# Kernel optimization log

Hardware: AMD Instinct MI355X
Metric: run time of the kernel (lower is better)

## Reference

```python
import jax, jax.numpy as jnp
import numpy as np

B, CIN, COUT = 2, 64, 64
D, H, W = 8, 32, 32
KD = KH = KW = 3
K = KD * KH * KW  # 27
STRIDE, PAD, DIL = 1, 1, 1
DOUT = (D + 2 * PAD - DIL * (KD - 1) - 1) // STRIDE + 1
HOUT = (H + 2 * PAD - DIL * (KH - 1) - 1) // STRIDE + 1
WOUT = (W + 2 * PAD - DIL * (KW - 1) - 1) // STRIDE + 1


def setup_inputs() -> dict:
    key = jax.random.key(0)
    k1, k2, k3, k4 = jax.random.split(key, 4)
    x = jax.random.normal(k1, (B, CIN, D, H, W), dtype=jnp.float32)
    offset = jax.random.normal(k2, (B, 3 * K, DOUT, HOUT, WOUT), dtype=jnp.float32)
    weight = jax.random.normal(k3, (COUT, CIN, KD, KH, KW), dtype=jnp.float32) * 0.05
    bias = jax.random.normal(k4, (COUT,), dtype=jnp.float32) * 0.1
    return {"x": x, "offset": offset, "weight": weight, "bias": bias}


def _trilinear_sample(xb, zd, zh, zw):
    # xb: [C, D, H, W]; zd/zh/zw: [K, P] float sampling coords (zero padding outside)
    Dd, Hh, Ww = xb.shape[1], xb.shape[2], xb.shape[3]
    d0 = jnp.floor(zd); h0 = jnp.floor(zh); w0 = jnp.floor(zw)
    fd = zd - d0; fh = zh - h0; fw = zw - w0
    d0i = d0.astype(jnp.int32); h0i = h0.astype(jnp.int32); w0i = w0.astype(jnp.int32)
    acc = jnp.zeros((xb.shape[0],) + zd.shape, dtype=xb.dtype)
    for dd in (0, 1):
        for dh in (0, 1):
            for dw in (0, 1):
                di = d0i + dd; hi = h0i + dh; wi = w0i + dw
                wgt = ((fd if dd else 1.0 - fd) * (fh if dh else 1.0 - fh)
                       * (fw if dw else 1.0 - fw))
                valid = ((di >= 0) & (di < Dd) & (hi >= 0) & (hi < Hh)
                         & (wi >= 0) & (wi < Ww)).astype(xb.dtype)
                v = xb[:, jnp.clip(di, 0, Dd - 1), jnp.clip(hi, 0, Hh - 1),
                       jnp.clip(wi, 0, Ww - 1)]  # [C, K, P]
                acc = acc + v * (wgt * valid)[None]
    return acc


def _deform_conv3d(x, offset, weight, bias):
    Bb = x.shape[0]
    P = DOUT * HOUT * WOUT
    # kernel taps
    kd, kh, kw = jnp.unravel_index(jnp.arange(K), (KD, KH, KW))
    # output grid
    od, oh, ow = jnp.meshgrid(jnp.arange(DOUT), jnp.arange(HOUT), jnp.arange(WOUT), indexing="ij")
    base_d = (od[None] * STRIDE - PAD + kd[:, None, None, None] * DIL).astype(jnp.float32)  # [K,Do,Ho,Wo]
    base_h = (oh[None] * STRIDE - PAD + kh[:, None, None, None] * DIL).astype(jnp.float32)
    base_w = (ow[None] * STRIDE - PAD + kw[:, None, None, None] * DIL).astype(jnp.float32)
    off = offset.reshape(Bb, K, 3, DOUT, HOUT, WOUT)  # per-tap (dd, dh, dw)
    zd = (base_d[None] + off[:, :, 0]).reshape(Bb, K, P)
    zh = (base_h[None] + off[:, :, 1]).reshape(Bb, K, P)
    zw = (base_w[None] + off[:, :, 2]).reshape(Bb, K, P)
    sampled = jax.vmap(_trilinear_sample)(x, zd, zh, zw)  # [B, C, K, P]
    wmat = weight.reshape(COUT, CIN, K)
    out = jnp.einsum("bckp,ock->bop", sampled, wmat)  # [B, COUT, P]
    out = out + bias[None, :, None]
    return out.reshape(Bb, COUT, DOUT, HOUT, WOUT)


def reference(x, offset, weight, bias):
    return _deform_conv3d(x, offset, weight, bias)
```

## Files before the change

### kernel.cpp

```cpp
#include <hip/hip_runtime.h>
#include <hip/hip_bf16.h>


#define BB    2
#define CINC  64
#define COUTC 64
#define DDEP  8
#define HGT   32
#define WID   32
#define KK    27
#define KGRP  3
#define KPG   9
#define KPH   3
#define PP    8192
#define TP    64
#define LDW   72

typedef short s16x8 __attribute__((ext_vector_type(8)));
typedef float f32x4 __attribute__((ext_vector_type(4)));

__device__ __forceinline__ unsigned short f2bf(float f) {
    unsigned u = __builtin_bit_cast(unsigned, f);
    u += 0x7FFFu + ((u >> 16) & 1u);
    return (unsigned short)(u >> 16);
}

__device__ __forceinline__ unsigned pack2bf(float lo, float hi) {
    return (unsigned)f2bf(lo) | ((unsigned)f2bf(hi) << 16);
}

__device__ __forceinline__ float bfu_lo(unsigned v) {
    return __builtin_bit_cast(float, v << 16);
}
__device__ __forceinline__ float bfu_hi(unsigned v) {
    return __builtin_bit_cast(float, v & 0xFFFF0000u);
}

__global__ void pre_kernel(const float* __restrict__ x, const float* __restrict__ w,
                           unsigned short* __restrict__ xt, unsigned short* __restrict__ wt) {
    __shared__ float sT[64][65];
    const int t    = threadIdx.x;
    const int lane = t & 63;
    const int wv   = t >> 6;
    const int half = lane >> 5;
    const int c2   = lane & 31;
    int blk = blockIdx.x;
    if (blk < 256) {
        int b  = blk >> 7;
        int s0 = (blk & 127) * 64;
        #pragma unroll
        for (int i = 0; i < 16; ++i) {
            int c = wv * 16 + i;
            sT[c][lane] = x[(size_t)(b * CINC + c) * PP + s0 + lane];
        }
        __syncthreads();
        #pragma unroll
        for (int i = 0; i < 8; ++i) {
            int s = wv * 16 + 2 * i + half;
            unsigned pk = pack2bf(sT[2 * c2][s], sT[2 * c2 + 1][s]);
            *(unsigned*)&xt[(size_t)(b * PP + s0 + s) * 64 + 2 * c2] = pk;
        }
    } else {
        int id = (blk - 256) * 256 + t;
        if (id < KK * COUTC * CINC) {
            int c = id & 63;
            int o = (id >> 6) & 63;
            int k = id >> 12;
            wt[id] = f2bf(w[(o * CINC + c) * KK + k]);
        }
    }
}

__global__ __launch_bounds__(256, 3) void deform_kernel(
    const unsigned short* __restrict__ xt, const float* __restrict__ off,
    const unsigned short* __restrict__ wt, const float* __restrict__ bias,
    float* __restrict__ out)
{
    __shared__ unsigned short sW[KPH * COUTC * LDW] __attribute__((aligned(16)));
    __shared__ unsigned short sS[TP * LDW]          __attribute__((aligned(16)));
    __shared__ int   sIdx[KPH][TP][8] __attribute__((aligned(16)));
    __shared__ float sCf[KPH][TP][8]  __attribute__((aligned(16)));

    const int t    = threadIdx.x;
    const int lane = t & 63;
    const int wv   = t >> 6;
    const int half = lane >> 5;
    const int c2   = lane & 31;
    const int b    = blockIdx.x >> 7;
    const int p0   = (blockIdx.x & 127) * TP;
    const int kg   = blockIdx.y;

    const unsigned short* xb = xt + (size_t)b * PP * 64;

    f32x4 acc[4];
    #pragma unroll
    for (int f = 0; f < 4; ++f) acc[f] = (f32x4)0.0f;

    const int n0 = lane & 15;
    const int q  = lane >> 4;

    #pragma unroll 1
    for (int ph = 0; ph < 3; ++ph) {
        const int kbase = kg * KPG + ph * KPH;

        const unsigned short* wk = wt + kbase * (COUTC * CINC);
        #pragma unroll
        for (int j = 0; j < 6; ++j) {
            int idx = j * 2048 + t * 8;
            int kl  = idx >> 12;
            int rem = idx & 4095;
            *(s16x8*)&sW[kl * (COUTC * LDW) + (rem >> 6) * LDW + (rem & 63)] =
                *(const s16x8*)(wk + idx);
        }

        if (t < KPH * TP) {
            int kl = t >> 6;
            int k  = kbase + kl;
            int pl = t & 63;
            int pp = p0 + pl;
            int ow = pp & 31;
            int oh = (pp >> 5) & 31;
            int od = pp >> 10;
            int kd = k / 9;
            int kh = (k - kd * 9) / 3;
            int kw = k - kd * 9 - kh * 3;
            const float* ob = off + (size_t)(b * (3 * KK) + 3 * k) * PP + pp;
            float zd = (float)(od - 1 + kd) + ob[0];
            float zh = (float)(oh - 1 + kh) + ob[PP];
            float zw = (float)(ow - 1 + kw) + ob[2 * PP];

            float fdf = floorf(zd); int d0 = (int)fdf; float fd = zd - fdf;
            float fhf = floorf(zh); int h0 = (int)fhf; float fh = zh - fhf;
            float fwf = floorf(zw); int w0 = (int)fwf; float fw = zw - fwf;

            float Bd0 = (d0 >= 0     && d0 < DDEP)     ? 1.0f - fd : 0.0f;
            float Bd1 = (d0 + 1 >= 0 && d0 + 1 < DDEP) ? fd        : 0.0f;
            float Ch0 = (h0 >= 0     && h0 < HGT)      ? 1.0f - fh : 0.0f;
            float Ch1 = (h0 + 1 >= 0 && h0 + 1 < HGT)  ? fh        : 0.0f;
            float Aw0 = (w0 >= 0     && w0 < WID)      ? 1.0f - fw : 0.0f;
            float Aw1 = (w0 + 1 >= 0 && w0 + 1 < WID)  ? fw        : 0.0f;
            int dc0 = min(max(d0, 0), DDEP - 1);
            int dc1 = min(max(d0 + 1, 0), DDEP - 1);
            int hc0 = min(max(h0, 0), HGT - 1);
            int hc1 = min(max(h0 + 1, 0), HGT - 1);
            int wc0 = min(max(w0, 0), WID - 1);
            int wc1 = min(max(w0 + 1, 0), WID - 1);

            int dhb0 = (dc0 * HGT + hc0) * (WID * 64);
            int dhb1 = (dc0 * HGT + hc1) * (WID * 64);
            int dhb2 = (dc1 * HGT + hc0) * (WID * 64);
            int dhb3 = (dc1 * HGT + hc1) * (WID * 64);
            int wo0 = wc0 * 64, wo1 = wc1 * 64;
            sIdx[kl][pl][0] = dhb0 + wo0;
            sIdx[kl][pl][1] = dhb1 + wo0;
            sIdx[kl][pl][2] = dhb2 + wo0;
            sIdx[kl][pl][3] = dhb3 + wo0;
            sIdx[kl][pl][4] = dhb0 + wo1;
            sIdx[kl][pl][5] = dhb1 + wo1;
            sIdx[kl][pl][6] = dhb2 + wo1;
            sIdx[kl][pl][7] = dhb3 + wo1;
            float bc0 = Bd0 * Ch0, bc1 = Bd0 * Ch1, bc2 = Bd1 * Ch0, bc3 = Bd1 * Ch1;
            sCf[kl][pl][0] = bc0 * Aw0;
            sCf[kl][pl][1] = bc1 * Aw0;
            sCf[kl][pl][2] = bc2 * Aw0;
            sCf[kl][pl][3] = bc3 * Aw0;
            sCf[kl][pl][4] = bc0 * Aw1;
            sCf[kl][pl][5] = bc1 * Aw1;
            sCf[kl][pl][6] = bc2 * Aw1;
            sCf[kl][pl][7] = bc3 * Aw1;
        }
        __syncthreads();

        #pragma unroll
        for (int kl = 0; kl < KPH; ++kl) {
            #pragma unroll
            for (int jp = 0; jp < 8; ++jp) {
                int prow = wv * 16 + 2 * jp + half;
                const int4   i0 = *(const int4*)&sIdx[kl][prow][0];
                const int4   i1 = *(const int4*)&sIdx[kl][prow][4];
                const float4 u0 = *(const float4*)&sCf[kl][prow][0];
                const float4 u1 = *(const float4*)&sCf[kl][prow][4];
                float slo = 0.0f, shi = 0.0f;
                {
                    unsigned v0 = *(const unsigned*)(xb + i0.x + 2 * c2);
                    unsigned v1 = *(const unsigned*)(xb + i0.y + 2 * c2);
                    unsigned v2 = *(const unsigned*)(xb + i0.z + 2 * c2);
                    unsigned v3 = *(const unsigned*)(xb + i0.w + 2 * c2);
                    unsigned v4 = *(const unsigned*)(xb + i1.x + 2 * c2);
                    unsigned v5 = *(const unsigned*)(xb + i1.y + 2 * c2);
                    unsigned v6 = *(const unsigned*)(xb + i1.z + 2 * c2);
                    unsigned v7 = *(const unsigned*)(xb + i1.w + 2 * c2);
                    slo += u0.x * bfu_lo(v0); shi += u0.x * bfu_hi(v0);
                    slo += u0.y * bfu_lo(v1); shi += u0.y * bfu_hi(v1);
                    slo += u0.z * bfu_lo(v2); shi += u0.z * bfu_hi(v2);
                    slo += u0.w * bfu_lo(v3); shi += u0.w * bfu_hi(v3);
                    slo += u1.x * bfu_lo(v4); shi += u1.x * bfu_hi(v4);
                    slo += u1.y * bfu_lo(v5); shi += u1.y * bfu_hi(v5);
                    slo += u1.z * bfu_lo(v6); shi += u1.z * bfu_hi(v6);
                    slo += u1.w * bfu_lo(v7); shi += u1.w * bfu_hi(v7);
                }
                *(unsigned*)&sS[prow * LDW + 2 * c2] = pack2bf(slo, shi);
            }
            __syncthreads();

            {
                const unsigned short* sWk = &sW[kl * (COUTC * LDW)];
                s16x8 a0 = *(const s16x8*)&sWk[(16 * wv + n0) * LDW +      8 * q];
                s16x8 a1 = *(const s16x8*)&sWk[(16 * wv + n0) * LDW + 32 + 8 * q];
                #pragma unroll
                for (int f = 0; f < 4; ++f) {
                    s16x8 b0 = *(const s16x8*)&sS[(16 * f + n0) * LDW +      8 * q];
                    s16x8 b1 = *(const s16x8*)&sS[(16 * f + n0) * LDW + 32 + 8 * q];
                    acc[f] = __builtin_amdgcn_mfma_f32_16x16x32_bf16(a0, b0, acc[f], 0, 0, 0);
                    acc[f] = __builtin_amdgcn_mfma_f32_16x16x32_bf16(a1, b1, acc[f], 0, 0, 0);
                }
            }
            __syncthreads();
        }
    }

    float bv[4];
    #pragma unroll
    for (int r = 0; r < 4; ++r) bv[r] = (kg == 0) ? bias[16 * wv + 4 * q + r] : 0.0f;
    #pragma unroll
    for (int f = 0; f < 4; ++f) {
        #pragma unroll
        for (int r = 0; r < 4; ++r) {
            int o = 16 * wv + 4 * q + r;
            int p = p0 + 16 * f + n0;
            unsafeAtomicAdd(&out[(size_t)(b * COUTC + o) * PP + p], acc[f][r] + bv[r]);
        }
    }
}

extern "C" void kernel_launch(void* const* d_in, const int* in_sizes, int n_in,
                              void* d_out, int out_size, void* d_ws, size_t ws_size,
                              hipStream_t stream) {
    const float* x    = (const float*)d_in[0];
    const float* off  = (const float*)d_in[1];
    const float* w    = (const float*)d_in[2];
    const float* bias = (const float*)d_in[3];
    float* out        = (float*)d_out;

    unsigned short* xt = (unsigned short*)d_ws;
    unsigned short* wt = (unsigned short*)((char*)d_ws + (size_t)BB * PP * 64 * 2);

    (void)hipMemsetAsync(out, 0, (size_t)out_size * sizeof(float), stream);
    hipLaunchKernelGGL(pre_kernel, dim3(256 + (KK * COUTC * CINC + 255) / 256), dim3(256), 0,
                       stream, x, w, xt, wt);
    hipLaunchKernelGGL(deform_kernel, dim3(BB * (PP / TP), KGRP), dim3(256), 0, stream,
                       xt, off, wt, bias, out);
}
```

Baseline: 103.3 us.

## Make sampling and MFMA wave-local, drop barriers, fold output zeroing into prekernel

Each wave now computes the offset coefficients, the trilinear samples and the MFMA for its own 16 output points, looping over all output-channel groups. The intra-phase __syncthreads between the sampling stage and the MFMA stage are removed; one barrier at the top of each phase still protects the weight reload. The separate hipMemsetAsync is replaced by extra zeroing blocks in pre_kernel. Sampling uses packed f32x2 math and a v_cvt_pk_bf16_f32 instruction, and the MFMA section is wrapped in s_setprio. The risk is that sW A-fragment LDS reads per MFMA rise, and the coefficient stage leaves a quarter of the lanes idle.

```diff
diff --git a/kernel.cpp b/kernel.cpp
--- a/kernel.cpp
+++ b/kernel.cpp
@@ -18,6 +18,7 @@
 
 typedef short s16x8 __attribute__((ext_vector_type(8)));
 typedef float f32x4 __attribute__((ext_vector_type(4)));
+typedef float f32x2 __attribute__((ext_vector_type(2)));
 
 __device__ __forceinline__ unsigned short f2bf(float f) {
     unsigned u = __builtin_bit_cast(unsigned, f);
@@ -29,15 +30,18 @@
     return (unsigned)f2bf(lo) | ((unsigned)f2bf(hi) << 16);
 }
 
-__device__ __forceinline__ float bfu_lo(unsigned v) {
-    return __builtin_bit_cast(float, v << 16);
-}
-__device__ __forceinline__ float bfu_hi(unsigned v) {
-    return __builtin_bit_cast(float, v & 0xFFFF0000u);
-}
-
+__device__ __forceinline__ f32x2 up2(unsigned v) {
+    f32x2 r;
+    r.x = __builtin_bit_cast(float, v << 16);
+    r.y = __builtin_bit_cast(float, v & 0xFFFF0000u);
+    return r;
+}
+
+#define WBLOCKS 432
+#define ZBLOCKS 1024
 __global__ void pre_kernel(const float* __restrict__ x, const float* __restrict__ w,
-                           unsigned short* __restrict__ xt, unsigned short* __restrict__ wt) {
+                           unsigned short* __restrict__ xt, unsigned short* __restrict__ wt,
+                           float* __restrict__ out) {
     __shared__ float sT[64][65];
     const int t    = threadIdx.x;
     const int lane = t & 63;
@@ -60,7 +64,7 @@
             unsigned pk = pack2bf(sT[2 * c2][s], sT[2 * c2 + 1][s]);
             *(unsigned*)&xt[(size_t)(b * PP + s0 + s) * 64 + 2 * c2] = pk;
         }
-    } else {
+    } else if (blk < 256 + WBLOCKS) {
         int id = (blk - 256) * 256 + t;
         if (id < KK * COUTC * CINC) {
             int c = id & 63;
@@ -68,6 +72,9 @@
             int k = id >> 12;
             wt[id] = f2bf(w[(o * CINC + c) * KK + k]);
         }
+    } else {
+        int id = (blk - 256 - WBLOCKS) * 256 + t;
+        ((float4*)out)[id] = make_float4(0.f, 0.f, 0.f, 0.f);
     }
 }
 
@@ -90,18 +97,23 @@
     const int p0   = (blockIdx.x & 127) * TP;
     const int kg   = blockIdx.y;
 
-    const unsigned short* xb = xt + (size_t)b * PP * 64;
+    const unsigned short* xb  = xt + (size_t)b * PP * 64;
+    const unsigned short* xbl = xb + 2 * c2;
 
     f32x4 acc[4];
     #pragma unroll
-    for (int f = 0; f < 4; ++f) acc[f] = (f32x4)0.0f;
-
-    const int n0 = lane & 15;
-    const int q  = lane >> 4;
+    for (int g = 0; g < 4; ++g) acc[g] = (f32x4)0.0f;
+
+    const int n0  = lane & 15;
+    const int q   = lane >> 4;
+    const int cr  = lane & 15;
+    const int ckl = lane >> 4;
 
     #pragma unroll 1
     for (int ph = 0; ph < 3; ++ph) {
         const int kbase = kg * KPG + ph * KPH;
+
+        __syncthreads();
 
         const unsigned short* wk = wt + kbase * (COUTC * CINC);
         #pragma unroll
@@ -113,10 +125,9 @@
                 *(const s16x8*)(wk + idx);
         }
 
-        if (t < KPH * TP) {
-            int kl = t >> 6;
-            int k  = kbase + kl;
-            int pl = t & 63;
+        if (ckl < KPH) {
+            int k  = kbase + ckl;
+            int pl = 16 * wv + cr;
             int pp = p0 + pl;
             int ow = pp & 31;
             int oh = (pp >> 5) & 31;
@@ -151,23 +162,23 @@
             int dhb2 = (dc1 * HGT + hc0) * (WID * 64);
             int dhb3 = (dc1 * HGT + hc1) * (WID * 64);
             int wo0 = wc0 * 64, wo1 = wc1 * 64;
-            sIdx[kl][pl][0] = dhb0 + wo0;
-            sIdx[kl][pl][1] = dhb1 + wo0;
-            sIdx[kl][pl][2] = dhb2 + wo0;
-            sIdx[kl][pl][3] = dhb3 + wo0;
-            sIdx[kl][pl][4] = dhb0 + wo1;
-            sIdx[kl][pl][5] = dhb1 + wo1;
-            sIdx[kl][pl][6] = dhb2 + wo1;
-            sIdx[kl][pl][7] = dhb3 + wo1;
+            sIdx[ckl][pl][0] = dhb0 + wo0;
+            sIdx[ckl][pl][1] = dhb1 + wo0;
+            sIdx[ckl][pl][2] = dhb2 + wo0;
+            sIdx[ckl][pl][3] = dhb3 + wo0;
+            sIdx[ckl][pl][4] = dhb0 + wo1;
+            sIdx[ckl][pl][5] = dhb1 + wo1;
+            sIdx[ckl][pl][6] = dhb2 + wo1;
+            sIdx[ckl][pl][7] = dhb3 + wo1;
             float bc0 = Bd0 * Ch0, bc1 = Bd0 * Ch1, bc2 = Bd1 * Ch0, bc3 = Bd1 * Ch1;
-            sCf[kl][pl][0] = bc0 * Aw0;
-            sCf[kl][pl][1] = bc1 * Aw0;
-            sCf[kl][pl][2] = bc2 * Aw0;
-            sCf[kl][pl][3] = bc3 * Aw0;
-            sCf[kl][pl][4] = bc0 * Aw1;
-            sCf[kl][pl][5] = bc1 * Aw1;
-            sCf[kl][pl][6] = bc2 * Aw1;
-            sCf[kl][pl][7] = bc3 * Aw1;
+            sCf[ckl][pl][0] = bc0 * Aw0;
+            sCf[ckl][pl][1] = bc1 * Aw0;
+            sCf[ckl][pl][2] = bc2 * Aw0;
+            sCf[ckl][pl][3] = bc3 * Aw0;
+            sCf[ckl][pl][4] = bc0 * Aw1;
+            sCf[ckl][pl][5] = bc1 * Aw1;
+            sCf[ckl][pl][6] = bc2 * Aw1;
+            sCf[ckl][pl][7] = bc3 * Aw1;
         }
         __syncthreads();
 
@@ -175,60 +186,59 @@
         for (int kl = 0; kl < KPH; ++kl) {
             #pragma unroll
             for (int jp = 0; jp < 8; ++jp) {
-                int prow = wv * 16 + 2 * jp + half;
+                int prow = 16 * wv + 2 * jp + half;
                 const int4   i0 = *(const int4*)&sIdx[kl][prow][0];
                 const int4   i1 = *(const int4*)&sIdx[kl][prow][4];
                 const float4 u0 = *(const float4*)&sCf[kl][prow][0];
                 const float4 u1 = *(const float4*)&sCf[kl][prow][4];
-                float slo = 0.0f, shi = 0.0f;
-                {
-                    unsigned v0 = *(const unsigned*)(xb + i0.x + 2 * c2);
-                    unsigned v1 = *(const unsigned*)(xb + i0.y + 2 * c2);
-                    unsigned v2 = *(const unsigned*)(xb + i0.z + 2 * c2);
-                    unsigned v3 = *(const unsigned*)(xb + i0.w + 2 * c2);
-                    unsigned v4 = *(const unsigned*)(xb + i1.x + 2 * c2);
-                    unsigned v5 = *(const unsigned*)(xb + i1.y + 2 * c2);
-                    unsigned v6 = *(const unsigned*)(xb + i1.z + 2 * c2);
-                    unsigned v7 = *(const unsigned*)(xb + i1.w + 2 * c2);
-                    slo += u0.x * bfu_lo(v0); shi += u0.x * bfu_hi(v0);
-                    slo += u0.y * bfu_lo(v1); shi += u0.y * bfu_hi(v1);
-                    slo += u0.z * bfu_lo(v2); shi += u0.z * bfu_hi(v2);
-                    slo += u0.w * bfu_lo(v3); shi += u0.w * bfu_hi(v3);
-                    slo += u1.x * bfu_lo(v4); shi += u1.x * bfu_hi(v4);
-                    slo += u1.y * bfu_lo(v5); shi += u1.y * bfu_hi(v5);
-                    slo += u1.z * bfu_lo(v6); shi += u1.z * bfu_hi(v6);
-                    slo += u1.w * bfu_lo(v7); shi += u1.w * bfu_hi(v7);
-                }
-                *(unsigned*)&sS[prow * LDW + 2 * c2] = pack2bf(slo, shi);
+                unsigned v0 = *(const unsigned*)(xbl + i0.x);
+                unsigned v1 = *(const unsigned*)(xbl + i0.y);
+                unsigned v2 = *(const unsigned*)(xbl + i0.z);
+                unsigned v3 = *(const unsigned*)(xbl + i0.w);
+                unsigned v4 = *(const unsigned*)(xbl + i1.x);
+                unsigned v5 = *(const unsigned*)(xbl + i1.y);
+                unsigned v6 = *(const unsigned*)(xbl + i1.z);
+                unsigned v7 = *(const unsigned*)(xbl + i1.w);
+                f32x2 s = {0.0f, 0.0f};
+                s += up2(v0) * u0.x;
+                s += up2(v1) * u0.y;
+                s += up2(v2) * u0.z;
+                s += up2(v3) * u0.w;
+                s += up2(v4) * u1.x;
+                s += up2(v5) * u1.y;
+                s += up2(v6) * u1.z;
+                s += up2(v7) * u1.w;
+                unsigned pkv;
+                asm("v_cvt_pk_bf16_f32 %0, %1, %2" : "=v"(pkv) : "v"(s.x), "v"(s.y));
+                *(unsigned*)&sS[prow * LDW + 2 * c2] = pkv;
             }
-            __syncthreads();
 
             {
                 const unsigned short* sWk = &sW[kl * (COUTC * LDW)];
-                s16x8 a0 = *(const s16x8*)&sWk[(16 * wv + n0) * LDW +      8 * q];
-                s16x8 a1 = *(const s16x8*)&sWk[(16 * wv + n0) * LDW + 32 + 8 * q];
+                s16x8 b0 = *(const s16x8*)&sS[(16 * wv + n0) * LDW +      8 * q];
+                s16x8 b1 = *(const s16x8*)&sS[(16 * wv + n0) * LDW + 32 + 8 * q];
+                __builtin_amdgcn_s_setprio(1);
                 #pragma unroll
-                for (int f = 0; f < 4; ++f) {
-                    s16x8 b0 = *(const s16x8*)&sS[(16 * f + n0) * LDW +      8 * q];
-                    s16x8 b1 = *(const s16x8*)&sS[(16 * f + n0) * LDW + 32 + 8 * q];
-                    acc[f] = __builtin_amdgcn_mfma_f32_16x16x32_bf16(a0, b0, acc[f], 0, 0, 0);
-                    acc[f] = __builtin_amdgcn_mfma_f32_16x16x32_bf16(a1, b1, acc[f], 0, 0, 0);
+                for (int g = 0; g < 4; ++g) {
+                    s16x8 a0 = *(const s16x8*)&sWk[(16 * g + n0) * LDW +      8 * q];
+                    s16x8 a1 = *(const s16x8*)&sWk[(16 * g + n0) * LDW + 32 + 8 * q];
+                    acc[g] = __builtin_amdgcn_mfma_f32_16x16x32_bf16(a0, b0, acc[g], 0, 0, 0);
+                    acc[g] = __builtin_amdgcn_mfma_f32_16x16x32_bf16(a1, b1, acc[g], 0, 0, 0);
                 }
+                __builtin_amdgcn_s_setprio(0);
             }
-            __syncthreads();
         }
     }
 
-    float bv[4];
+    const int p = p0 + 16 * wv + n0;
     #pragma unroll
-    for (int r = 0; r < 4; ++r) bv[r] = (kg == 0) ? bias[16 * wv + 4 * q + r] : 0.0f;
-    #pragma unroll
-    for (int f = 0; f < 4; ++f) {
+    for (int g = 0; g < 4; ++g) {
         #pragma unroll
         for (int r = 0; r < 4; ++r) {
-            int o = 16 * wv + 4 * q + r;
-            int p = p0 + 16 * f + n0;
-            unsafeAtomicAdd(&out[(size_t)(b * COUTC + o) * PP + p], acc[f][r] + bv[r]);
+            int o = 16 * g + 4 * q + r;
+            float v = acc[g][r];
+            if (kg == 0) v += bias[o];
+            unsafeAtomicAdd(&out[(size_t)(b * COUTC + o) * PP + p], v);
         }
     }
 }
@@ -245,9 +255,8 @@
     unsigned short* xt = (unsigned short*)d_ws;
     unsigned short* wt = (unsigned short*)((char*)d_ws + (size_t)BB * PP * 64 * 2);
 
-    (void)hipMemsetAsync(out, 0, (size_t)out_size * sizeof(float), stream);
-    hipLaunchKernelGGL(pre_kernel, dim3(256 + (KK * COUTC * CINC + 255) / 256), dim3(256), 0,
-                       stream, x, w, xt, wt);
+    hipLaunchKernelGGL(pre_kernel, dim3(256 + WBLOCKS + ZBLOCKS), dim3(256), 0,
+                       stream, x, w, xt, wt, out);
     hipLaunchKernelGGL(deform_kernel, dim3(BB * (PP / TP), KGRP), dim3(256), 0, stream,
                        xt, off, wt, bias, out);
 }
```

Measured after the change: 100.4 us. 1.03x faster.
